# Kernel tuning notes

Measured on AMD Instinct MI355X. Metric: run time of the kernel, lower is better.

Reference implementation:

```python
import jax, jax.numpy as jnp
import numpy as np

STEPS = 8         # Euler integration steps (module arg `steps`)
ALPHA = 1e-2      # membrane (Laplacian) weight of the Riemannian metric
GAMMA = 1e-3      # absolute displacement weight (keeps metric invertible)


def _l_hat(spatial, dtype):
    """Fourier transfer function of L = gamma + alpha * (-discrete Laplacian).

    Circulant boundary conditions -> diagonal in Fourier space.
    Returns array broadcastable over the spatial dims, shape == spatial.
    """
    nd = len(spatial)
    lap = None
    for i, n in enumerate(spatial):
        k = jnp.arange(n, dtype=dtype)
        t = 2.0 - 2.0 * jnp.cos(2.0 * jnp.pi * k / n)
        shape = [1] * nd
        shape[i] = n
        t = t.reshape(shape)
        lap = t if lap is None else lap + t
    return GAMMA + ALPHA * lap


def _pullback(f, disp, grid):
    """Sample f at x + disp(x) with trilinear interpolation, wrap boundary.

    f:    [B, C, X, Y, Z]  field to pull back
    disp: [B, D, X, Y, Z]  voxel displacement (D == number of spatial dims)
    grid: [D, X, Y, Z]     identity coordinate grid
    """
    coords = grid[None] + disp  # [B, D, X, Y, Z]
    nd = grid.shape[0]

    def samp(channel, co):  # channel: [X,Y,Z], co: [D,X,Y,Z]
        return jax.scipy.ndimage.map_coordinates(
            channel, [co[d] for d in range(nd)], order=1, mode='wrap')

    # vmap over batch, then over channels (coords shared across channels)
    return jax.vmap(lambda fb, cb: jax.vmap(lambda ch: samp(ch, cb))(fb))(f, coords)


def _shoot(v):
    """Geodesic shooting of initial velocity v: [B, D, *spatial] -> phi (disp).

    m0 = L v0 (momentum); each Euler step: v = K m, compose phi with dt*v,
    transport momentum by pullback (fast scheme, no Jacobian correction).
    """
    spatial = v.shape[2:]
    axes = tuple(range(-len(spatial), 0))
    lh = _l_hat(spatial, v.dtype)

    def L(x):
        return jnp.fft.ifftn(jnp.fft.fftn(x, axes=axes) * lh, axes=axes).real.astype(v.dtype)

    def K(x):
        return jnp.fft.ifftn(jnp.fft.fftn(x, axes=axes) / lh, axes=axes).real.astype(v.dtype)

    grid = jnp.stack(jnp.meshgrid(
        *[jnp.arange(n, dtype=v.dtype) for n in spatial], indexing='ij'))  # [D, X, Y, Z]

    dt = 1.0 / STEPS
    m0 = L(v)
    phi0 = jnp.zeros_like(v)

    def step(carry, _):
        phi, m = carry
        sv = dt * K(m)                        # small velocity for this step
        phi = _pullback(phi, sv, grid) + sv   # phi <- phi o (id + dt*v)
        m = _pullback(m, sv, grid)            # fast momentum transport
        return (phi, m), None

    (phi, _), _ = jax.lax.scan(step, (phi0, m0), None, length=STEPS)
    return phi


def setup_inputs() -> dict:
    key = jax.random.key(0)
    v = 0.5 * jax.random.normal(key, (2, 3, 128, 128, 128), dtype=jnp.float32)
    return {"v": v}


def reference(v) -> jnp.ndarray:
    # Module does movedim(1,-1) -> shoot -> movedim(-1,1); we keep the
    # channels-first layout throughout, which is mathematically identical.
    return _shoot(v)
```

## Files before the change

### kernel.cpp

```cpp
#include <hip/hip_runtime.h>
#include <math.h>

#define VV (128*128*128)

#define K_GAMMA 1e-3f
#define K_ALPHA 1e-2f
#define K_DTN3  5.9604644775390625e-08f
#define K_W0    0.04908738521234052f

__device__ __forceinline__ void sh_fwd(float& rlo, float& ilo, float& rhi, float& ihi,
                                       const int lane,
                                       const float* __restrict__ twr,
                                       const float* __restrict__ twi) {
  {
    const float wr = twr[lane], ws = twi[lane];
    const float dr = rlo - rhi, di = ilo - ihi;
    rlo += rhi;  ilo += ihi;
    rhi = dr * wr + di * ws;
    ihi = di * wr - dr * ws;
  }
#pragma unroll
  for (int lh = 5; lh >= 0; --lh) {
    const int h  = 1 << lh;
    const int up = lane & h;
    const int ti = (lane & (h - 1)) << (6 - lh);
    const float wr = twr[ti], ws = twi[ti];
    float pr = __shfl_xor(rlo, h), pi = __shfl_xor(ilo, h);
    float dr = up ? (pr - rlo) : (rlo + pr);
    float di = up ? (pi - ilo) : (ilo + pi);
    rlo = up ? (dr * wr + di * ws) : dr;
    ilo = up ? (di * wr - dr * ws) : di;
    pr = __shfl_xor(rhi, h);  pi = __shfl_xor(ihi, h);
    dr = up ? (pr - rhi) : (rhi + pr);
    di = up ? (pi - ihi) : (ihi + pi);
    rhi = up ? (dr * wr + di * ws) : dr;
    ihi = up ? (di * wr - dr * ws) : di;
  }
}

__device__ __forceinline__ void sh_inv(float& rlo, float& ilo, float& rhi, float& ihi,
                                       const int lane,
                                       const float* __restrict__ twr,
                                       const float* __restrict__ twi) {
#pragma unroll
  for (int lh = 0; lh <= 5; ++lh) {
    const int h  = 1 << lh;
    const int up = lane & h;
    const int ti = (lane & (h - 1)) << (6 - lh);
    const float wr = twr[ti], ws = twi[ti];
    float pr = __shfl_xor(rlo, h), pi = __shfl_xor(ilo, h);
    float ar = up ? pr : rlo,  ai = up ? pi : ilo;
    float br = up ? rlo : pr,  bi = up ? ilo : pi;
    float cr = br * wr - bi * ws, ci = br * ws + bi * wr;
    rlo = up ? (ar - cr) : (ar + cr);
    ilo = up ? (ai - ci) : (ai + ci);
    pr = __shfl_xor(rhi, h);  pi = __shfl_xor(ihi, h);
    ar = up ? pr : rhi;  ai = up ? pi : ihi;
    br = up ? rhi : pr;  bi = up ? ihi : pi;
    cr = br * wr - bi * ws;  ci = br * ws + bi * wr;
    rhi = up ? (ar - cr) : (ar + cr);
    ihi = up ? (ai - ci) : (ai + ci);
  }
  {
    const float wr = twr[lane], ws = twi[lane];
    const float cr = rhi * wr - ihi * ws, ci = rhi * ws + ihi * wr;
    rhi = rlo - cr;  ihi = ilo - ci;
    rlo += cr;       ilo += ci;
  }
}

__global__ __launch_bounds__(256) void k_stencil_L(const float* __restrict__ v,
                                                   float* __restrict__ m) {
  const int idx = blockIdx.x * 256 + threadIdx.x;
  const int vox = idx & (VV - 1);
  const int r   = idx >> 21;
  const int z = vox & 127, y = (vox >> 7) & 127, x = vox >> 14;
  const float* base = v + (size_t)r * VV;
  const float c = base[vox];
  const int xm = (x - 1) & 127, xp = (x + 1) & 127;
  const int ym = (y - 1) & 127, yp = (y + 1) & 127;
  const int zm = (z - 1) & 127, zp = (z + 1) & 127;
  const float nsum = base[(xm << 14) | (y << 7) | z] + base[(xp << 14) | (y << 7) | z]
                   + base[(x << 14) | (ym << 7) | z] + base[(x << 14) | (yp << 7) | z]
                   + base[(x << 14) | (y << 7) | zm] + base[(x << 14) | (y << 7) | zp];
  m[idx] = K_GAMMA * c + K_ALPHA * (6.0f * c - nsum);
}

__global__ __launch_bounds__(1024) void k_fft_zy_f(const float* __restrict__ m,
                                                   float2* __restrict__ cbuf) {
  __shared__ float twr[64], twi[64];
  __shared__ float s_re[128 * 129], s_im[128 * 129];
  const int tid = threadIdx.x, lane = tid & 63, wv = tid >> 6;
  if (tid < 64) {
    float s, c; sincosf((float)tid * K_W0, &s, &c);
    twr[tid] = c; twi[tid] = s;
  }
  const int p = blockIdx.x >> 7, x = blockIdx.x & 127;
  const float* r0 = m + (size_t)(2 * p) * VV + (size_t)x * 16384;
  const float* r1 = r0 + VV;
  float rlo[8], ilo[8], rhi[8], ihi[8];
#pragma unroll
  for (int l = 0; l < 8; ++l) {
    const int row = ((wv << 3) | l) << 7;
    rlo[l] = r0[row + lane];  rhi[l] = r0[row + lane + 64];
    ilo[l] = r1[row + lane];  ihi[l] = r1[row + lane + 64];
  }
  __syncthreads();
#pragma unroll
  for (int l = 0; l < 8; ++l) {
    sh_fwd(rlo[l], ilo[l], rhi[l], ihi[l], lane, twr, twi);
    const int y = (wv << 3) | l;
    s_re[y * 129 + lane] = rlo[l];  s_re[y * 129 + lane + 64] = rhi[l];
    s_im[y * 129 + lane] = ilo[l];  s_im[y * 129 + lane + 64] = ihi[l];
  }
  __syncthreads();
#pragma unroll
  for (int l = 0; l < 8; ++l) {
    const int z = (wv << 3) | l;
    float arl = s_re[lane * 129 + z],        ail = s_im[lane * 129 + z];
    float arh = s_re[(lane + 64) * 129 + z], aih = s_im[(lane + 64) * 129 + z];
    sh_fwd(arl, ail, arh, aih, lane, twr, twi);
    s_re[lane * 129 + z] = arl;  s_re[(lane + 64) * 129 + z] = arh;
    s_im[lane * 129 + z] = ail;  s_im[(lane + 64) * 129 + z] = aih;
  }
  __syncthreads();
  float2* cb = cbuf + (size_t)p * VV + (size_t)x * 16384;
#pragma unroll
  for (int i = 0; i < 16; ++i) {
    const int e = tid + i * 1024, y = e >> 7, z = e & 127;
    cb[e] = make_float2(s_re[y * 129 + z], s_im[y * 129 + z]);
  }
}

__global__ __launch_bounds__(1024) void k_fft_zy_i(float2* __restrict__ cbuf) {
  __shared__ float twr[64], twi[64];
  __shared__ float s_re[128 * 129], s_im[128 * 129];
  const int tid = threadIdx.x, lane = tid & 63, wv = tid >> 6;
  if (tid < 64) {
    float s, c; sincosf((float)tid * K_W0, &s, &c);
    twr[tid] = c; twi[tid] = s;
  }
  const int p = blockIdx.x >> 7, x = blockIdx.x & 127;
  float2* cb = cbuf + (size_t)p * VV + (size_t)x * 16384;
#pragma unroll
  for (int i = 0; i < 16; ++i) {
    const int e = tid + i * 1024, y = e >> 7, z = e & 127;
    const float2 v = cb[e];
    s_re[y * 129 + z] = v.x;  s_im[y * 129 + z] = v.y;
  }
  __syncthreads();
#pragma unroll
  for (int l = 0; l < 8; ++l) {
    const int z = (wv << 3) | l;
    float arl = s_re[lane * 129 + z],        ail = s_im[lane * 129 + z];
    float arh = s_re[(lane + 64) * 129 + z], aih = s_im[(lane + 64) * 129 + z];
    sh_inv(arl, ail, arh, aih, lane, twr, twi);
    s_re[lane * 129 + z] = arl;  s_re[(lane + 64) * 129 + z] = arh;
    s_im[lane * 129 + z] = ail;  s_im[(lane + 64) * 129 + z] = aih;
  }
  __syncthreads();
#pragma unroll
  for (int l = 0; l < 8; ++l) {
    const int y = (wv << 3) | l;
    float arl = s_re[y * 129 + lane],      ail = s_im[y * 129 + lane];
    float arh = s_re[y * 129 + lane + 64], aih = s_im[y * 129 + lane + 64];
    sh_inv(arl, ail, arh, aih, lane, twr, twi);
    cb[(y << 7) + lane]      = make_float2(arl, ail);
    cb[(y << 7) + lane + 64] = make_float2(arh, aih);
  }
}

__global__ __launch_bounds__(512) void k_fft_x_fused(float2* __restrict__ cbuf) {
  __shared__ float twr[64], twi[64], tt[128];
  __shared__ float s_re[128 * 17], s_im[128 * 17];
  const int tid = threadIdx.x, lane = tid & 63, wv = tid >> 6;
  if (tid < 64) {
    float s, c; sincosf((float)tid * K_W0, &s, &c);
    twr[tid] = c; twi[tid] = s;
  }
  if (tid < 128) {
    const int br = (int)(__brev((unsigned)tid) >> 25);
    tt[tid] = 2.0f - 2.0f * cosf((float)br * K_W0);
  }
  const int bid = blockIdx.x;
  const int p = bid >> 10, rem = bid & 1023;
  const int y = rem >> 3, z0 = (rem & 7) << 4;
  float2* base = cbuf + (size_t)p * VV + (size_t)(y * 128 + z0);
#pragma unroll
  for (int i = 0; i < 4; ++i) {
    const int e = tid + i * 512, xx = e >> 4, zz = e & 15;
    const float2 v = base[(size_t)xx * 16384 + zz];
    s_re[xx * 17 + zz] = v.x;  s_im[xx * 17 + zz] = v.y;
  }
  __syncthreads();
  const float tyv = tt[y];
#pragma unroll
  for (int l = 0; l < 2; ++l) {
    const int zz = wv + (l << 3);
    float arl = s_re[lane * 17 + zz],        ail = s_im[lane * 17 + zz];
    float arh = s_re[(lane + 64) * 17 + zz], aih = s_im[(lane + 64) * 17 + zz];
    sh_fwd(arl, ail, arh, aih, lane, twr, twi);
    const float tzv = tt[z0 + zz];
    const float slo = K_DTN3 / (K_GAMMA + K_ALPHA * (tt[lane] + tyv + tzv));
    const float shi = K_DTN3 / (K_GAMMA + K_ALPHA * (tt[lane + 64] + tyv + tzv));
    arl *= slo;  ail *= slo;  arh *= shi;  aih *= shi;
    sh_inv(arl, ail, arh, aih, lane, twr, twi);
    s_re[lane * 17 + zz] = arl;  s_re[(lane + 64) * 17 + zz] = arh;
    s_im[lane * 17 + zz] = ail;  s_im[(lane + 64) * 17 + zz] = aih;
  }
  __syncthreads();
#pragma unroll
  for (int i = 0; i < 4; ++i) {
    const int e = tid + i * 512, xx = e >> 4, zz = e & 15;
    base[(size_t)xx * 16384 + zz] = make_float2(s_re[xx * 17 + zz], s_im[xx * 17 + zz]);
  }
}

__global__ __launch_bounds__(256, 2) void k_pullback(const float* __restrict__ svc,
                                                     const float* __restrict__ phiA,
                                                     const float* __restrict__ mA,
                                                     float* __restrict__ phiB,
                                                     float* __restrict__ mB) {
  const int idx = blockIdx.x * 256 + threadIdx.x;
  const int b   = idx >> 21;
  const int vox = idx & (VV - 1);
  const int z = vox & 127, y = (vox >> 7) & 127, x = vox >> 14;
  const int r0 = b * 3;
  const float d0 = svc[(size_t)((r0)     >> 1) * 2 * VV + ((size_t)vox << 1) + ((r0)     & 1)];
  const float d1 = svc[(size_t)((r0 + 1) >> 1) * 2 * VV + ((size_t)vox << 1) + ((r0 + 1) & 1)];
  const float d2 = svc[(size_t)((r0 + 2) >> 1) * 2 * VV + ((size_t)vox << 1) + ((r0 + 2) & 1)];
  const float cx = (float)x + d0, cy = (float)y + d1, cz = (float)z + d2;
  const float flx = floorf(cx), fly = floorf(cy), flz = floorf(cz);
  const float wx = cx - flx, wy = cy - fly, wz = cz - flz;
  const int x0 = ((int)flx) & 127, y0 = ((int)fly) & 127, z0 = ((int)flz) & 127;
  const int x1 = (x0 + 1) & 127,  y1 = (y0 + 1) & 127,  z1 = (z0 + 1) & 127;
  int o[8];
  o[0] = (x0 * 128 + y0) * 128 + z0;  o[1] = (x0 * 128 + y0) * 128 + z1;
  o[2] = (x0 * 128 + y1) * 128 + z0;  o[3] = (x0 * 128 + y1) * 128 + z1;
  o[4] = (x1 * 128 + y0) * 128 + z0;  o[5] = (x1 * 128 + y0) * 128 + z1;
  o[6] = (x1 * 128 + y1) * 128 + z0;  o[7] = (x1 * 128 + y1) * 128 + z1;
  const size_t sb = (size_t)b * 3 * VV;
  float g[6][8];
#pragma unroll
  for (int c = 0; c < 3; ++c) {
    const float* P = phiA + sb + (size_t)c * VV;
#pragma unroll
    for (int k = 0; k < 8; ++k) g[c][k] = P[o[k]];
  }
#pragma unroll
  for (int c = 0; c < 3; ++c) {
    const float* M = mA + sb + (size_t)c * VV;
#pragma unroll
    for (int k = 0; k < 8; ++k) g[3 + c][k] = M[o[k]];
  }
  const float ux = 1.f - wx, uy = 1.f - wy, uz = 1.f - wz;
  float w[8];
  w[0] = ux * uy * uz;  w[1] = ux * uy * wz;
  w[2] = ux * wy * uz;  w[3] = ux * wy * wz;
  w[4] = wx * uy * uz;  w[5] = wx * uy * wz;
  w[6] = wx * wy * uz;  w[7] = wx * wy * wz;
  const float dd[3] = {d0, d1, d2};
#pragma unroll
  for (int c = 0; c < 3; ++c) {
    float sp = 0.f, sm = 0.f;
#pragma unroll
    for (int k = 0; k < 8; ++k) { sp += w[k] * g[c][k];  sm += w[k] * g[3 + c][k]; }
    phiB[sb + (size_t)c * VV + vox] = sp + dd[c];
    mB[sb + (size_t)c * VV + vox]   = sm;
  }
}

extern "C" void kernel_launch(void* const* d_in, const int* in_sizes, int n_in,
                              void* d_out, int out_size, void* d_ws, size_t ws_size,
                              hipStream_t stream) {
  (void)in_sizes; (void)n_in; (void)out_size; (void)ws_size;
  const float* v = (const float*)d_in[0];
  float* phi0 = (float*)d_out;
  float* ws   = (float*)d_ws;
  const size_t FV = (size_t)6 * VV;
  float* phi1 = ws;
  float* mA   = ws + FV;
  float* mB   = ws + 2 * FV;
  float2* cbuf = (float2*)(ws + 3 * FV);

  hipMemsetAsync(phi0, 0, FV * sizeof(float), stream);
  k_stencil_L<<<dim3((unsigned)(FV / 256)), dim3(256), 0, stream>>>(v, mA);

  float* phiA = phi0; float* phiB = phi1;
  float* ma = mA;     float* mb = mB;
  for (int s = 0; s < 8; ++s) {
    k_fft_zy_f<<<dim3(384), dim3(1024), 0, stream>>>(ma, cbuf);
    k_fft_x_fused<<<dim3(3072), dim3(512), 0, stream>>>(cbuf);
    k_fft_zy_i<<<dim3(384), dim3(1024), 0, stream>>>(cbuf);
    k_pullback<<<dim3(16384), dim3(256), 0, stream>>>((const float*)cbuf,
                                                      phiA, ma, phiB, mb);
    float* t = phiA; phiA = phiB; phiB = t;
    t = ma; ma = mb; mb = t;
  }
}
```

Before: 2.418 ms.

## Tile pullback with shared-memory halo for interpolation stencil reuse

Measured after the change: 2.136 ms. 11.7% less time.

```diff
diff --git a/kernel.cpp b/kernel.cpp
--- a/kernel.cpp
+++ b/kernel.cpp
@@ -216,57 +216,99 @@
   }
 }
 
-__global__ __launch_bounds__(256, 2) void k_pullback(const float* __restrict__ svc,
-                                                     const float* __restrict__ phiA,
-                                                     const float* __restrict__ mA,
-                                                     float* __restrict__ phiB,
-                                                     float* __restrict__ mB) {
-  const int idx = blockIdx.x * 256 + threadIdx.x;
-  const int b   = idx >> 21;
-  const int vox = idx & (VV - 1);
-  const int z = vox & 127, y = (vox >> 7) & 127, x = vox >> 14;
-  const int r0 = b * 3;
-  const float d0 = svc[(size_t)((r0)     >> 1) * 2 * VV + ((size_t)vox << 1) + ((r0)     & 1)];
-  const float d1 = svc[(size_t)((r0 + 1) >> 1) * 2 * VV + ((size_t)vox << 1) + ((r0 + 1) & 1)];
-  const float d2 = svc[(size_t)((r0 + 2) >> 1) * 2 * VV + ((size_t)vox << 1) + ((r0 + 2) & 1)];
-  const float cx = (float)x + d0, cy = (float)y + d1, cz = (float)z + d2;
-  const float flx = floorf(cx), fly = floorf(cy), flz = floorf(cz);
-  const float wx = cx - flx, wy = cy - fly, wz = cz - flz;
-  const int x0 = ((int)flx) & 127, y0 = ((int)fly) & 127, z0 = ((int)flz) & 127;
-  const int x1 = (x0 + 1) & 127,  y1 = (y0 + 1) & 127,  z1 = (z0 + 1) & 127;
-  int o[8];
-  o[0] = (x0 * 128 + y0) * 128 + z0;  o[1] = (x0 * 128 + y0) * 128 + z1;
-  o[2] = (x0 * 128 + y1) * 128 + z0;  o[3] = (x0 * 128 + y1) * 128 + z1;
-  o[4] = (x1 * 128 + y0) * 128 + z0;  o[5] = (x1 * 128 + y0) * 128 + z1;
-  o[6] = (x1 * 128 + y1) * 128 + z0;  o[7] = (x1 * 128 + y1) * 128 + z1;
+__global__ __launch_bounds__(256) void k_pullback_t(const float* __restrict__ svc,
+                                                    const float* __restrict__ phiA,
+                                                    const float* __restrict__ mA,
+                                                    float* __restrict__ phiB,
+                                                    float* __restrict__ mB) {
+  __shared__ float2 TP[3][6][6][36];
+  __shared__ float  S[3][512];
+  const int tid = threadIdx.x;
+  const int bid = blockIdx.x;
+  const int b  = bid >> 12;
+  const int rr = bid & 4095;
+  const int X = ((rr >> 7) & 31) << 2;
+  const int Y = ((rr >> 2) & 31) << 2;
+  const int Z = (rr & 3) << 5;
   const size_t sb = (size_t)b * 3 * VV;
-  float g[6][8];
-#pragma unroll
-  for (int c = 0; c < 3; ++c) {
-    const float* P = phiA + sb + (size_t)c * VV;
-#pragma unroll
-    for (int k = 0; k < 8; ++k) g[c][k] = P[o[k]];
-  }
-#pragma unroll
-  for (int c = 0; c < 3; ++c) {
-    const float* M = mA + sb + (size_t)c * VV;
-#pragma unroll
-    for (int k = 0; k < 8; ++k) g[3 + c][k] = M[o[k]];
-  }
-  const float ux = 1.f - wx, uy = 1.f - wy, uz = 1.f - wz;
-  float w[8];
-  w[0] = ux * uy * uz;  w[1] = ux * uy * wz;
-  w[2] = ux * wy * uz;  w[3] = ux * wy * wz;
-  w[4] = wx * uy * uz;  w[5] = wx * uy * wz;
-  w[6] = wx * wy * uz;  w[7] = wx * wy * wz;
-  const float dd[3] = {d0, d1, d2};
-#pragma unroll
-  for (int c = 0; c < 3; ++c) {
-    float sp = 0.f, sm = 0.f;
-#pragma unroll
-    for (int k = 0; k < 8; ++k) { sp += w[k] * g[c][k];  sm += w[k] * g[3 + c][k]; }
-    phiB[sb + (size_t)c * VV + vox] = sp + dd[c];
-    mB[sb + (size_t)c * VV + vox]   = sm;
+  for (int j = tid; j < 3 * 1296; j += 256) {
+    const int cp  = j / 1296;
+    const int rm  = j - cp * 1296;
+    const int rx  = rm / 216;
+    const int rm2 = rm - rx * 216;
+    const int ry  = rm2 / 36;
+    const int rz  = rm2 - ry * 36;
+    const int g = (((X - 1 + rx) & 127) << 14) | (((Y - 1 + ry) & 127) << 7)
+                | ((Z - 1 + rz) & 127);
+    TP[cp][rx][ry][rz] = make_float2(phiA[sb + (size_t)cp * VV + g],
+                                     mA[sb + (size_t)cp * VV + g]);
+  }
+  for (int j = tid; j < 1536; j += 256) {
+    const int c = j >> 9, v = j & 511;
+    const int slz = v & 31, sly = (v >> 5) & 3, slx = v >> 7;
+    const int g = ((X + slx) << 14) | ((Y + sly) << 7) | (Z + slz);
+    const int rch = b * 3 + c;
+    S[c][v] = svc[(size_t)(rch >> 1) * 2 * VV + ((size_t)g << 1) + (rch & 1)];
+  }
+  __syncthreads();
+  const int lz = tid & 31, ly = (tid >> 5) & 3, lx0 = tid >> 7;
+#pragma unroll
+  for (int q = 0; q < 2; ++q) {
+    const int lx = lx0 + (q << 1);
+    const int v  = (lx << 7) | (ly << 5) | lz;
+    const float d0 = S[0][v], d1 = S[1][v], d2 = S[2][v];
+    const int gx = X + lx, gy = Y + ly, gz = Z + lz;
+    const float cx = (float)gx + d0, cy = (float)gy + d1, cz = (float)gz + d2;
+    const float flx = floorf(cx), fly = floorf(cy), flz = floorf(cz);
+    const float wx = cx - flx, wy = cy - fly, wz = cz - flz;
+    const float ux = 1.f - wx, uy = 1.f - wy, uz = 1.f - wz;
+    const float w000 = ux * uy * uz, w001 = ux * uy * wz;
+    const float w010 = ux * wy * uz, w011 = ux * wy * wz;
+    const float w100 = wx * uy * uz, w101 = wx * uy * wz;
+    const float w110 = wx * wy * uz, w111 = wx * wy * wz;
+    const int x0l = (int)flx - (X - 1);
+    const int y0l = (int)fly - (Y - 1);
+    const int z0l = (int)flz - (Z - 1);
+    const int g = (gx << 14) | (gy << 7) | gz;
+    const float dd[3] = {d0, d1, d2};
+    if ((unsigned)x0l <= 4u && (unsigned)y0l <= 4u && (unsigned)z0l <= 32u) {
+#pragma unroll
+      for (int cp = 0; cp < 3; ++cp) {
+        const float2 c000 = TP[cp][x0l][y0l][z0l];
+        const float2 c001 = TP[cp][x0l][y0l][z0l + 1];
+        const float2 c010 = TP[cp][x0l][y0l + 1][z0l];
+        const float2 c011 = TP[cp][x0l][y0l + 1][z0l + 1];
+        const float2 c100 = TP[cp][x0l + 1][y0l][z0l];
+        const float2 c101 = TP[cp][x0l + 1][y0l][z0l + 1];
+        const float2 c110 = TP[cp][x0l + 1][y0l + 1][z0l];
+        const float2 c111 = TP[cp][x0l + 1][y0l + 1][z0l + 1];
+        const float sp = w000 * c000.x + w001 * c001.x + w010 * c010.x + w011 * c011.x
+                       + w100 * c100.x + w101 * c101.x + w110 * c110.x + w111 * c111.x;
+        const float sm = w000 * c000.y + w001 * c001.y + w010 * c010.y + w011 * c011.y
+                       + w100 * c100.y + w101 * c101.y + w110 * c110.y + w111 * c111.y;
+        phiB[sb + (size_t)cp * VV + g] = sp + dd[cp];
+        mB[sb + (size_t)cp * VV + g]   = sm;
+      }
+    } else {
+      const int xg0 = ((int)flx) & 127, yg0 = ((int)fly) & 127, zg0 = ((int)flz) & 127;
+      const int xg1 = (xg0 + 1) & 127, yg1 = (yg0 + 1) & 127, zg1 = (zg0 + 1) & 127;
+      int o[8];
+      o[0] = (xg0 * 128 + yg0) * 128 + zg0;  o[1] = (xg0 * 128 + yg0) * 128 + zg1;
+      o[2] = (xg0 * 128 + yg1) * 128 + zg0;  o[3] = (xg0 * 128 + yg1) * 128 + zg1;
+      o[4] = (xg1 * 128 + yg0) * 128 + zg0;  o[5] = (xg1 * 128 + yg0) * 128 + zg1;
+      o[6] = (xg1 * 128 + yg1) * 128 + zg0;  o[7] = (xg1 * 128 + yg1) * 128 + zg1;
+      const float w[8] = {w000, w001, w010, w011, w100, w101, w110, w111};
+#pragma unroll
+      for (int cp = 0; cp < 3; ++cp) {
+        const float* P = phiA + sb + (size_t)cp * VV;
+        const float* M = mA + sb + (size_t)cp * VV;
+        float sp = 0.f, sm = 0.f;
+#pragma unroll
+        for (int k = 0; k < 8; ++k) { sp += w[k] * P[o[k]]; sm += w[k] * M[o[k]]; }
+        phiB[sb + (size_t)cp * VV + g] = sp + dd[cp];
+        mB[sb + (size_t)cp * VV + g]   = sm;
+      }
+    }
   }
 }
 
@@ -292,8 +334,8 @@
     k_fft_zy_f<<<dim3(384), dim3(1024), 0, stream>>>(ma, cbuf);
     k_fft_x_fused<<<dim3(3072), dim3(512), 0, stream>>>(cbuf);
     k_fft_zy_i<<<dim3(384), dim3(1024), 0, stream>>>(cbuf);
-    k_pullback<<<dim3(16384), dim3(256), 0, stream>>>((const float*)cbuf,
-                                                      phiA, ma, phiB, mb);
+    k_pullback_t<<<dim3(8192), dim3(256), 0, stream>>>((const float*)cbuf,
+                                                       phiA, ma, phiB, mb);
     float* t = phiA; phiA = phiB; phiB = t;
     t = ma; ma = mb; mb = t;
   }
```
